# Optimization experiments

Measured on AMD Instinct MI355X. Metric: run time of the kernel, lower is better.

The kernel has to match this reference:

```python
import jax, jax.numpy as jnp
import numpy as np

B, L, C = 8, 256, 64
NEG = -1e30  # large negative instead of -inf to keep grads NaN-free


def setup_inputs() -> dict:
    key = jax.random.key(0)
    k1, k2 = jax.random.split(key)
    scores = jax.random.normal(k1, (B, L, L, C), dtype=jnp.float32)
    lens = jax.random.randint(k2, (B,), 64, L, dtype=jnp.int32)  # sentence lengths in [64, L-1]
    return {"scores": scores, "lens": lens}


def _inside_max(scores, lens):
    """Max-semiring CKY inside pass. scores: [B,L,L,C]; returns logZ per batch [B]."""
    t = jnp.transpose(jnp.max(scores, axis=-1), (1, 2, 0))  # [L,L,B] best label per span
    s0 = jnp.zeros((L, L, B), scores.dtype)                 # chart s[i,j] = best score of span (i,j)
    i = jnp.arange(L)
    j = jnp.arange(L)

    def step(s, w):
        e = jnp.clip(i + w, 0, L - 1)                       # span end, [L]
        k = jnp.clip(i[:, None] + j[None, :], 0, L - 1)     # split points, [L,L]
        left = s[i[:, None], k]                             # s[i, i+j], [L,L,B]
        right = s[k, e[:, None]]                            # s[i+j, i+w], [L,L,B]
        valid = (j[None, :] >= 1) & (j[None, :] < w) & ((i + w) < L)[:, None]
        comb = jnp.max(jnp.where(valid[..., None], left + right, NEG), axis=1)  # [L,B]
        s_l = t[i, e]                                       # label-max span score, [L,B]
        diag = jnp.where(w == 1, s_l, comb + s_l)
        row_ok = ((i + w) < L)[:, None]
        upd = jnp.where(row_ok, diag, s[i, e])
        s = s.at[i, e].set(upd)
        return s, None

    s, _ = jax.lax.scan(step, s0, jnp.arange(1, L))
    lens_c = jnp.clip(lens, 1, L - 1)
    return s[0, lens_c, jnp.arange(B)]                      # logZ (best tree score) per sentence


def reference(scores, lens):
    return _inside_max(scores, lens)
```

## Files before the change

kernel.cpp:

```cpp
#include <hip/hip_runtime.h>

#define LVAL 256
#define T    32
#define ST   36
#define SLAB (T * ST)
#define NB   8
#define NEG  (-1e30f)

#define LDS_FENCE() asm volatile("s_waitcnt lgkmcnt(0)" ::: "memory")

__device__ __forceinline__ size_t sidx(int b, int i, int e) {
    return ((size_t)b << 16) + (i << 8) + e;
}

template<int CTRL>
__device__ __forceinline__ float dpp_max(float v) {
#if __has_builtin(__builtin_amdgcn_mov_dpp)
    int o = __builtin_amdgcn_mov_dpp(__builtin_bit_cast(int, v), CTRL, 0xF, 0xF, true);
    return fmaxf(v, __builtin_bit_cast(float, o));
#else
    return fmaxf(v, __shfl_xor(v, CTRL == 0xB1 ? 1 : 2));
#endif
}

__global__ __launch_bounds__(256) void phase1(const float* __restrict__ scores,
                                              float* __restrict__ s) {
    const int i = blockIdx.x, b = blockIdx.y;
    const int sub = threadIdx.x & 15, slot = threadIdx.x >> 4;
    const float* row = scores + ((((size_t)b * LVAL + i) * LVAL) << 6);
    #pragma unroll 4
    for (int m0 = 0; m0 < LVAL; m0 += 16) {
        const int e = m0 + slot;
        if (e > i) {
            float4 v = *((const float4*)(row + ((size_t)e << 6)) + sub);
            float mx = fmaxf(fmaxf(v.x, v.y), fmaxf(v.z, v.w));
            #pragma unroll
            for (int d = 1; d < 16; d <<= 1) mx = fmaxf(mx, __shfl_xor(mx, d));
            if (sub == 0) s[sidx(b, i, e)] = mx;
        }
    }
}

template<int LP>
__device__ __forceinline__ void diag_step(int lane, int l,
                                          float (*cur)[ST], float (*curT)[ST],
                                          const float (*tb)[ST]) {
    const int cells = T - l;
    const int P = 1 << LP;
    const int c = lane >> LP, p = lane & (P - 1);
    const bool guard = c < cells;
    const int li = guard ? c : 0;
    const int le = guard ? c + l : 0;
    constexpr int NF = 8 >> LP;
    const float tv = tb[li][le];
    float acc = NEG;
    #pragma unroll
    for (int m = 0; m < NF; ++m) {
        const int k0 = 4 * (p + m * P);
        float4 cu = *(const float4*)&cur[li][k0];
        float4 ct = *(const float4*)&curT[le][k0];
        acc = fmaxf(acc, fmaxf(fmaxf(cu.x + ct.x, cu.y + ct.y),
                               fmaxf(cu.z + ct.z, cu.w + ct.w)));
    }
    acc = dpp_max<0xB1>(acc);
    if (LP >= 2) acc = dpp_max<0x4E>(acc);
    const float v = acc + tv;
    if (guard && p == 0) cur[li][le] = v;
    if (guard && p == 1) curT[le][li] = v;
}

__global__ __launch_bounds__(64) void round0(float* __restrict__ s) {
    __shared__ __align__(16) float curS[SLAB], curTS[SLAB], tbS[SLAB];
    float (*cur)[ST]  = (float(*)[ST])curS;
    float (*curT)[ST] = (float(*)[ST])curTS;
    float (*tb)[ST]   = (float(*)[ST])tbS;
    const int bi = blockIdx.x & 7, b = blockIdx.x >> 3;
    const int lane = threadIdx.x;
    const int row = lane >> 1, ch = (lane & 1) * 16;
    const float4 negv = make_float4(NEG, NEG, NEG, NEG);
    #pragma unroll
    for (int j = 0; j < 4; ++j) {
        float4 v = *(const float4*)&s[sidx(b, bi * T + row, bi * T + ch + 4 * j)];
        *(float4*)&tb[row][ch + 4 * j]   = v;
        *(float4*)&cur[row][ch + 4 * j]  = negv;
        *(float4*)&curT[row][ch + 4 * j] = negv;
    }
    LDS_FENCE();
    if (lane < T - 1) {
        float v = tb[lane][lane + 1];
        cur[lane][lane + 1] = v;
        curT[lane + 1][lane] = v;
    }
    LDS_FENCE();
    #pragma unroll 1
    for (int l = 2; l < T; ++l) {
        if (T - l <= 16) diag_step<2>(lane, l, cur, curT, tb);
        else             diag_step<1>(lane, l, cur, curT, tb);
        LDS_FENCE();
    }
    #pragma unroll
    for (int j = 0; j < 4; ++j)
        *(float4*)&s[sidx(b, bi * T + row, bi * T + ch + 4 * j)] =
            *(const float4*)&cur[row][ch + 4 * j];
}

template<int LP>
__device__ __forceinline__ void edge_step(int lane, int l, int D,
                                          const float (*Ae)[ST], const float (*BeT)[ST],
                                          float (*cur)[ST], float (*curT)[ST],
                                          const float (*tb)[ST], const float (*pre)[ST]) {
    const int delta = l - (T - 1);
    const int ad = delta < 0 ? -delta : delta;
    const int cells = T - ad;
    const int P = 1 << LP;
    const int c = lane >> LP, p = lane & (P - 1);
    const bool guard = c < cells;
    const int li = guard ? (delta < 0 ? c + ad : c) : 0;
    const int le = guard ? li + delta : 0;
    constexpr int NF = 8 >> LP;
    const float tv = tb[li][le];
    float acc = pre[li][le];
    #pragma unroll
    for (int m = 0; m < NF; ++m) {
        const int k0 = 4 * (p + m * P);
        float4 a  = *(const float4*)&Ae[li][k0];
        float4 ct = *(const float4*)&curT[le][k0];
        float4 cu = *(const float4*)&cur[li][k0];
        float4 bt = *(const float4*)&BeT[le][k0];
        float s0 = fmaxf(fmaxf(a.x + ct.x, a.y + ct.y), fmaxf(a.z + ct.z, a.w + ct.w));
        float s1 = fmaxf(fmaxf(cu.x + bt.x, cu.y + bt.y), fmaxf(cu.z + bt.z, cu.w + bt.w));
        acc = fmaxf(acc, fmaxf(s0, s1));
    }
    acc = dpp_max<0xB1>(acc);
    if (LP >= 2) acc = dpp_max<0x4E>(acc);
    const float v = (D == 1 && l == 0) ? tv : acc + tv;
    if (guard && p == 0) cur[li][le] = v;
    if (guard && p == 1) curT[le][li] = v;
}

__global__ __launch_bounds__(256) void roundD(float* __restrict__ s, int D,
                                              const int* __restrict__ lens,
                                              float* __restrict__ out) {
    __shared__ __align__(16) float smem[14 * SLAB];
    float (*Ae)[ST]   = (float(*)[ST])(smem + 0 * SLAB);
    float (*BeT)[ST]  = (float(*)[ST])(smem + 1 * SLAB);
    float (*cur)[ST]  = (float(*)[ST])(smem + 2 * SLAB);
    float (*curT)[ST] = (float(*)[ST])(smem + 3 * SLAB);
    float (*tb)[ST]   = (float(*)[ST])(smem + 4 * SLAB);
    float (*pre)[ST]  = (float(*)[ST])(smem + 5 * SLAB);
    float* ATb = smem + 6 * SLAB;
    float* BWb = smem + 10 * SLAB;

    const int nbi = NB - D;
    const int b = blockIdx.x / nbi, bi = blockIdx.x % nbi, be = bi + D;
    const int tid = threadIdx.x, wid = tid >> 6, lane = tid & 63;
    const int lr = tid >> 5, lc = tid & 31;
    const int grow = lane >> 1, gc = (lane & 1) * 16;
    const int gly = lane >> 3, glx = lane & 7, r0 = 4 * gly, c0 = 4 * glx;
    const int nw = (D - 1 < 4) ? (D - 1) : 4;
    float (*AT)[ST] = (float(*)[ST])(ATb + wid * SLAB);
    float (*BW)[ST] = (float(*)[ST])(BWb + wid * SLAB);

    float ag[4][4];
    #pragma unroll
    for (int i = 0; i < 4; ++i)
        #pragma unroll
        for (int j = 0; j < 4; ++j) ag[i][j] = NEG;
    for (int K = bi + 1 + wid; K < be; K += 4) {
        #pragma unroll
        for (int j = 0; j < 4; ++j) {
            float4 av = *(const float4*)&s[sidx(b, bi * T + grow, K * T + gc + 4 * j)];
            AT[gc + 4 * j + 0][grow] = av.x;
            AT[gc + 4 * j + 1][grow] = av.y;
            AT[gc + 4 * j + 2][grow] = av.z;
            AT[gc + 4 * j + 3][grow] = av.w;
            float4 bv = *(const float4*)&s[sidx(b, K * T + grow, be * T + gc + 4 * j)];
            *(float4*)&BW[grow][gc + 4 * j] = bv;
        }
        LDS_FENCE();
        #pragma unroll 4
        for (int k = 0; k < T; ++k) {
            float4 a4 = *(const float4*)&AT[k][r0];
            float4 b4 = *(const float4*)&BW[k][c0];
            const float aa[4] = {a4.x, a4.y, a4.z, a4.w};
            const float bb[4] = {b4.x, b4.y, b4.z, b4.w};
            #pragma unroll
            for (int i = 0; i < 4; ++i)
                #pragma unroll
                for (int j = 0; j < 4; ++j)
                    ag[i][j] = fmaxf(ag[i][j], aa[i] + bb[j]);
        }
        LDS_FENCE();
    }
    if (wid < nw) {
        #pragma unroll
        for (int i = 0; i < 4; ++i)
            *(float4*)&AT[r0 + i][c0] = make_float4(ag[i][0], ag[i][1], ag[i][2], ag[i][3]);
    }
    #pragma unroll
    for (int r = 0; r < 4; ++r) {
        const int row = lr + 8 * r;
        float va = s[sidx(b, bi * T + row, bi * T + lc)];
        Ae[row][lc] = (lc > row) ? va : NEG;
        float vb = s[sidx(b, be * T + row, be * T + lc)];
        BeT[lc][row] = (row < lc) ? vb : NEG;
        tb[row][lc] = s[sidx(b, bi * T + row, be * T + lc)];
        cur[row][lc] = NEG;
        curT[row][lc] = NEG;
    }
    __syncthreads();
    #pragma unroll
    for (int r = 0; r < 4; ++r) {
        const int row = lr + 8 * r;
        float v = NEG;
        for (int w2 = 0; w2 < nw; ++w2)
            v = fmaxf(v, ATb[w2 * SLAB + row * ST + lc]);
        pre[row][lc] = v;
    }
    __syncthreads();

    if (wid == 0) {
        #pragma unroll 1
        for (int l = 0; l < 2 * T - 1; ++l) {
            const int ad0 = (l < T - 1) ? (T - 1 - l) : (l - (T - 1));
            if (ad0 >= 16) edge_step<2>(lane, l, D, Ae, BeT, cur, curT, tb, pre);
            else           edge_step<1>(lane, l, D, Ae, BeT, cur, curT, tb, pre);
            LDS_FENCE();
        }
    }
    __syncthreads();
    #pragma unroll
    for (int r = 0; r < 4; ++r)
        s[sidx(b, bi * T + lr + 8 * r, be * T + lc)] = cur[lr + 8 * r][lc];

    if (D == NB - 1 && tid == 0) {
        int len = lens[b];
        len = len < 1 ? 1 : (len > LVAL - 1 ? LVAL - 1 : len);
        out[b] = (len >= (NB - 1) * T) ? cur[0][len - (NB - 1) * T]
                                       : s[sidx(b, 0, len)];
    }
}

extern "C" void kernel_launch(void* const* d_in, const int* in_sizes, int n_in,
                              void* d_out, int out_size, void* d_ws, size_t ws_size,
                              hipStream_t stream) {
    const float* scores = (const float*)d_in[0];
    const int*   lens   = (const int*)d_in[1];
    float*       out    = (float*)d_out;
    float*       s      = (float*)d_ws;

    phase1<<<dim3(LVAL, 8), 256, 0, stream>>>(scores, s);
    round0<<<64, 64, 0, stream>>>(s);
    for (int D = 1; D < NB; ++D)
        roundD<<<(NB - D) * 8, 256, 0, stream>>>(s, D, lens, out);
}
```

Baseline: 354.1 us.

## Fuse DP rounds into one cooperative kernel with grid syncs and trim edge loop

Replaces the round0 kernel and the seven roundD launches with a single cooperative kernel of 64 blocks that runs all rounds and separates them with grid.sync(). This removes per-launch overhead and the inter-kernel gaps in the serial chain of small kernels. It also adds a trimmed edge_step variant for early anti-diagonals that reads only the half of the split range known to be non-NEG, cutting LDS reads. The trade-off is that a cooperative launch needs every block resident at once, and blocks with no work in later rounds still wait at each grid barrier.

```diff
diff --git a/kernel.cpp b/kernel.cpp
--- a/kernel.cpp
+++ b/kernel.cpp
@@ -1,4 +1,7 @@
 #include <hip/hip_runtime.h>
+#include <hip/hip_cooperative_groups.h>
+
+namespace cg = cooperative_groups;
 
 #define LVAL 256
 #define T    32
@@ -69,42 +72,7 @@
     if (guard && p == 1) curT[le][li] = v;
 }
 
-__global__ __launch_bounds__(64) void round0(float* __restrict__ s) {
-    __shared__ __align__(16) float curS[SLAB], curTS[SLAB], tbS[SLAB];
-    float (*cur)[ST]  = (float(*)[ST])curS;
-    float (*curT)[ST] = (float(*)[ST])curTS;
-    float (*tb)[ST]   = (float(*)[ST])tbS;
-    const int bi = blockIdx.x & 7, b = blockIdx.x >> 3;
-    const int lane = threadIdx.x;
-    const int row = lane >> 1, ch = (lane & 1) * 16;
-    const float4 negv = make_float4(NEG, NEG, NEG, NEG);
-    #pragma unroll
-    for (int j = 0; j < 4; ++j) {
-        float4 v = *(const float4*)&s[sidx(b, bi * T + row, bi * T + ch + 4 * j)];
-        *(float4*)&tb[row][ch + 4 * j]   = v;
-        *(float4*)&cur[row][ch + 4 * j]  = negv;
-        *(float4*)&curT[row][ch + 4 * j] = negv;
-    }
-    LDS_FENCE();
-    if (lane < T - 1) {
-        float v = tb[lane][lane + 1];
-        cur[lane][lane + 1] = v;
-        curT[lane + 1][lane] = v;
-    }
-    LDS_FENCE();
-    #pragma unroll 1
-    for (int l = 2; l < T; ++l) {
-        if (T - l <= 16) diag_step<2>(lane, l, cur, curT, tb);
-        else             diag_step<1>(lane, l, cur, curT, tb);
-        LDS_FENCE();
-    }
-    #pragma unroll
-    for (int j = 0; j < 4; ++j)
-        *(float4*)&s[sidx(b, bi * T + row, bi * T + ch + 4 * j)] =
-            *(const float4*)&cur[row][ch + 4 * j];
-}
-
-template<int LP>
+template<int LP, int TRIM>
 __device__ __forceinline__ void edge_step(int lane, int l, int D,
                                           const float (*Ae)[ST], const float (*BeT)[ST],
                                           float (*cur)[ST], float (*curT)[ST],
@@ -117,19 +85,34 @@
     const bool guard = c < cells;
     const int li = guard ? (delta < 0 ? c + ad : c) : 0;
     const int le = guard ? li + delta : 0;
-    constexpr int NF = 8 >> LP;
     const float tv = tb[li][le];
     float acc = pre[li][le];
-    #pragma unroll
-    for (int m = 0; m < NF; ++m) {
-        const int k0 = 4 * (p + m * P);
-        float4 a  = *(const float4*)&Ae[li][k0];
-        float4 ct = *(const float4*)&curT[le][k0];
-        float4 cu = *(const float4*)&cur[li][k0];
-        float4 bt = *(const float4*)&BeT[le][k0];
-        float s0 = fmaxf(fmaxf(a.x + ct.x, a.y + ct.y), fmaxf(a.z + ct.z, a.w + ct.w));
-        float s1 = fmaxf(fmaxf(cu.x + bt.x, cu.y + bt.y), fmaxf(cu.z + bt.z, cu.w + bt.w));
-        acc = fmaxf(acc, fmaxf(s0, s1));
+    if (TRIM) {
+        constexpr int NF = 4 >> LP;
+        #pragma unroll
+        for (int m = 0; m < (NF ? NF : 1); ++m) {
+            const int kk = 4 * (p + m * P);
+            float4 a  = *(const float4*)&Ae[li][16 + kk];
+            float4 ct = *(const float4*)&curT[le][16 + kk];
+            float4 cu = *(const float4*)&cur[li][kk];
+            float4 bt = *(const float4*)&BeT[le][kk];
+            float s0 = fmaxf(fmaxf(a.x + ct.x, a.y + ct.y), fmaxf(a.z + ct.z, a.w + ct.w));
+            float s1 = fmaxf(fmaxf(cu.x + bt.x, cu.y + bt.y), fmaxf(cu.z + bt.z, cu.w + bt.w));
+            acc = fmaxf(acc, fmaxf(s0, s1));
+        }
+    } else {
+        constexpr int NF = 8 >> LP;
+        #pragma unroll
+        for (int m = 0; m < NF; ++m) {
+            const int k0 = 4 * (p + m * P);
+            float4 a  = *(const float4*)&Ae[li][k0];
+            float4 ct = *(const float4*)&curT[le][k0];
+            float4 cu = *(const float4*)&cur[li][k0];
+            float4 bt = *(const float4*)&BeT[le][k0];
+            float s0 = fmaxf(fmaxf(a.x + ct.x, a.y + ct.y), fmaxf(a.z + ct.z, a.w + ct.w));
+            float s1 = fmaxf(fmaxf(cu.x + bt.x, cu.y + bt.y), fmaxf(cu.z + bt.z, cu.w + bt.w));
+            acc = fmaxf(acc, fmaxf(s0, s1));
+        }
     }
     acc = dpp_max<0xB1>(acc);
     if (LP >= 2) acc = dpp_max<0x4E>(acc);
@@ -138,9 +121,9 @@
     if (guard && p == 1) curT[le][li] = v;
 }
 
-__global__ __launch_bounds__(256) void roundD(float* __restrict__ s, int D,
-                                              const int* __restrict__ lens,
-                                              float* __restrict__ out) {
+__global__ __launch_bounds__(256)
+void dp_coop(float* __restrict__ s, const int* __restrict__ lens,
+             float* __restrict__ out) {
     __shared__ __align__(16) float smem[14 * SLAB];
     float (*Ae)[ST]   = (float(*)[ST])(smem + 0 * SLAB);
     float (*BeT)[ST]  = (float(*)[ST])(smem + 1 * SLAB);
@@ -151,93 +134,139 @@
     float* ATb = smem + 6 * SLAB;
     float* BWb = smem + 10 * SLAB;
 
-    const int nbi = NB - D;
-    const int b = blockIdx.x / nbi, bi = blockIdx.x % nbi, be = bi + D;
+    cg::grid_group grid = cg::this_grid();
     const int tid = threadIdx.x, wid = tid >> 6, lane = tid & 63;
     const int lr = tid >> 5, lc = tid & 31;
     const int grow = lane >> 1, gc = (lane & 1) * 16;
     const int gly = lane >> 3, glx = lane & 7, r0 = 4 * gly, c0 = 4 * glx;
-    const int nw = (D - 1 < 4) ? (D - 1) : 4;
     float (*AT)[ST] = (float(*)[ST])(ATb + wid * SLAB);
     float (*BW)[ST] = (float(*)[ST])(BWb + wid * SLAB);
 
-    float ag[4][4];
-    #pragma unroll
-    for (int i = 0; i < 4; ++i)
-        #pragma unroll
-        for (int j = 0; j < 4; ++j) ag[i][j] = NEG;
-    for (int K = bi + 1 + wid; K < be; K += 4) {
-        #pragma unroll
-        for (int j = 0; j < 4; ++j) {
-            float4 av = *(const float4*)&s[sidx(b, bi * T + grow, K * T + gc + 4 * j)];
-            AT[gc + 4 * j + 0][grow] = av.x;
-            AT[gc + 4 * j + 1][grow] = av.y;
-            AT[gc + 4 * j + 2][grow] = av.z;
-            AT[gc + 4 * j + 3][grow] = av.w;
-            float4 bv = *(const float4*)&s[sidx(b, K * T + grow, be * T + gc + 4 * j)];
-            *(float4*)&BW[grow][gc + 4 * j] = bv;
-        }
-        LDS_FENCE();
-        #pragma unroll 4
-        for (int k = 0; k < T; ++k) {
-            float4 a4 = *(const float4*)&AT[k][r0];
-            float4 b4 = *(const float4*)&BW[k][c0];
-            const float aa[4] = {a4.x, a4.y, a4.z, a4.w};
-            const float bb[4] = {b4.x, b4.y, b4.z, b4.w};
+    {
+        const int bi = blockIdx.x & 7, b = blockIdx.x >> 3;
+        if (wid == 0) {
+            const int row = lane >> 1, ch = (lane & 1) * 16;
+            const float4 negv = make_float4(NEG, NEG, NEG, NEG);
+            #pragma unroll
+            for (int j = 0; j < 4; ++j) {
+                float4 v = *(const float4*)&s[sidx(b, bi * T + row, bi * T + ch + 4 * j)];
+                *(float4*)&tb[row][ch + 4 * j]   = v;
+                *(float4*)&cur[row][ch + 4 * j]  = negv;
+                *(float4*)&curT[row][ch + 4 * j] = negv;
+            }
+            LDS_FENCE();
+            if (lane < T - 1) {
+                float v = tb[lane][lane + 1];
+                cur[lane][lane + 1] = v;
+                curT[lane + 1][lane] = v;
+            }
+            LDS_FENCE();
+            #pragma unroll 1
+            for (int l = 2; l < T; ++l) {
+                if (T - l <= 16) diag_step<2>(lane, l, cur, curT, tb);
+                else             diag_step<1>(lane, l, cur, curT, tb);
+                LDS_FENCE();
+            }
+            #pragma unroll
+            for (int j = 0; j < 4; ++j)
+                *(float4*)&s[sidx(b, bi * T + row, bi * T + ch + 4 * j)] =
+                    *(const float4*)&cur[row][ch + 4 * j];
+        }
+        __syncthreads();
+    }
+    grid.sync();
+
+    for (int D = 1; D < NB; ++D) {
+        const int nbi = NB - D;
+        if (blockIdx.x < nbi * 8) {
+            const int b = blockIdx.x / nbi, bi = blockIdx.x % nbi, be = bi + D;
+            const int nw = (D - 1 < 4) ? (D - 1) : 4;
+
+            float ag[4][4];
             #pragma unroll
             for (int i = 0; i < 4; ++i)
                 #pragma unroll
-                for (int j = 0; j < 4; ++j)
-                    ag[i][j] = fmaxf(ag[i][j], aa[i] + bb[j]);
-        }
-        LDS_FENCE();
-    }
-    if (wid < nw) {
-        #pragma unroll
-        for (int i = 0; i < 4; ++i)
-            *(float4*)&AT[r0 + i][c0] = make_float4(ag[i][0], ag[i][1], ag[i][2], ag[i][3]);
-    }
-    #pragma unroll
-    for (int r = 0; r < 4; ++r) {
-        const int row = lr + 8 * r;
-        float va = s[sidx(b, bi * T + row, bi * T + lc)];
-        Ae[row][lc] = (lc > row) ? va : NEG;
-        float vb = s[sidx(b, be * T + row, be * T + lc)];
-        BeT[lc][row] = (row < lc) ? vb : NEG;
-        tb[row][lc] = s[sidx(b, bi * T + row, be * T + lc)];
-        cur[row][lc] = NEG;
-        curT[row][lc] = NEG;
-    }
-    __syncthreads();
-    #pragma unroll
-    for (int r = 0; r < 4; ++r) {
-        const int row = lr + 8 * r;
-        float v = NEG;
-        for (int w2 = 0; w2 < nw; ++w2)
-            v = fmaxf(v, ATb[w2 * SLAB + row * ST + lc]);
-        pre[row][lc] = v;
-    }
-    __syncthreads();
-
-    if (wid == 0) {
-        #pragma unroll 1
-        for (int l = 0; l < 2 * T - 1; ++l) {
-            const int ad0 = (l < T - 1) ? (T - 1 - l) : (l - (T - 1));
-            if (ad0 >= 16) edge_step<2>(lane, l, D, Ae, BeT, cur, curT, tb, pre);
-            else           edge_step<1>(lane, l, D, Ae, BeT, cur, curT, tb, pre);
-            LDS_FENCE();
-        }
-    }
-    __syncthreads();
-    #pragma unroll
-    for (int r = 0; r < 4; ++r)
-        s[sidx(b, bi * T + lr + 8 * r, be * T + lc)] = cur[lr + 8 * r][lc];
-
-    if (D == NB - 1 && tid == 0) {
-        int len = lens[b];
-        len = len < 1 ? 1 : (len > LVAL - 1 ? LVAL - 1 : len);
-        out[b] = (len >= (NB - 1) * T) ? cur[0][len - (NB - 1) * T]
-                                       : s[sidx(b, 0, len)];
+                for (int j = 0; j < 4; ++j) ag[i][j] = NEG;
+            for (int K = bi + 1 + wid; K < be; K += 4) {
+                #pragma unroll
+                for (int j = 0; j < 4; ++j) {
+                    float4 av = *(const float4*)&s[sidx(b, bi * T + grow, K * T + gc + 4 * j)];
+                    AT[gc + 4 * j + 0][grow] = av.x;
+                    AT[gc + 4 * j + 1][grow] = av.y;
+                    AT[gc + 4 * j + 2][grow] = av.z;
+                    AT[gc + 4 * j + 3][grow] = av.w;
+                    float4 bv = *(const float4*)&s[sidx(b, K * T + grow, be * T + gc + 4 * j)];
+                    *(float4*)&BW[grow][gc + 4 * j] = bv;
+                }
+                LDS_FENCE();
+                #pragma unroll 4
+                for (int k = 0; k < T; ++k) {
+                    float4 a4 = *(const float4*)&AT[k][r0];
+                    float4 b4 = *(const float4*)&BW[k][c0];
+                    const float aa[4] = {a4.x, a4.y, a4.z, a4.w};
+                    const float bb[4] = {b4.x, b4.y, b4.z, b4.w};
+                    #pragma unroll
+                    for (int i = 0; i < 4; ++i)
+                        #pragma unroll
+                        for (int j = 0; j < 4; ++j)
+                            ag[i][j] = fmaxf(ag[i][j], aa[i] + bb[j]);
+                }
+                LDS_FENCE();
+            }
+            if (wid < nw) {
+                #pragma unroll
+                for (int i = 0; i < 4; ++i)
+                    *(float4*)&AT[r0 + i][c0] =
+                        make_float4(ag[i][0], ag[i][1], ag[i][2], ag[i][3]);
+            }
+            #pragma unroll
+            for (int r = 0; r < 4; ++r) {
+                const int row = lr + 8 * r;
+                float va = s[sidx(b, bi * T + row, bi * T + lc)];
+                Ae[row][lc] = (lc > row) ? va : NEG;
+                float vb = s[sidx(b, be * T + row, be * T + lc)];
+                BeT[lc][row] = (row < lc) ? vb : NEG;
+                tb[row][lc] = s[sidx(b, bi * T + row, be * T + lc)];
+                cur[row][lc] = NEG;
+                curT[row][lc] = NEG;
+            }
+            __syncthreads();
+            #pragma unroll
+            for (int r = 0; r < 4; ++r) {
+                const int row = lr + 8 * r;
+                float v = NEG;
+                for (int w2 = 0; w2 < nw; ++w2)
+                    v = fmaxf(v, ATb[w2 * SLAB + row * ST + lc]);
+                pre[row][lc] = v;
+            }
+            __syncthreads();
+
+            if (wid == 0) {
+                #pragma unroll 1
+                for (int l = 0; l < 2 * T - 1; ++l) {
+                    const int ad0 = (l < T - 1) ? (T - 1 - l) : (l - (T - 1));
+                    if (l < T - 1 && ad0 >= 16)
+                        edge_step<2, 1>(lane, l, D, Ae, BeT, cur, curT, tb, pre);
+                    else if (ad0 >= 16)
+                        edge_step<2, 0>(lane, l, D, Ae, BeT, cur, curT, tb, pre);
+                    else
+                        edge_step<1, 0>(lane, l, D, Ae, BeT, cur, curT, tb, pre);
+                    LDS_FENCE();
+                }
+            }
+            __syncthreads();
+            #pragma unroll
+            for (int r = 0; r < 4; ++r)
+                s[sidx(b, bi * T + lr + 8 * r, be * T + lc)] = cur[lr + 8 * r][lc];
+
+            if (D == NB - 1 && tid == 0) {
+                int len = lens[b];
+                len = len < 1 ? 1 : (len > LVAL - 1 ? LVAL - 1 : len);
+                out[b] = (len >= (NB - 1) * T) ? cur[0][len - (NB - 1) * T]
+                                               : s[sidx(b, 0, len)];
+            }
+        }
+        grid.sync();
     }
 }
 
@@ -250,7 +279,7 @@
     float*       s      = (float*)d_ws;
 
     phase1<<<dim3(LVAL, 8), 256, 0, stream>>>(scores, s);
-    round0<<<64, 64, 0, stream>>>(s);
-    for (int D = 1; D < NB; ++D)
-        roundD<<<(NB - D) * 8, 256, 0, stream>>>(s, D, lens, out);
-}
+
+    void* args[] = {(void*)&s, (void*)&lens, (void*)&out};
+    hipLaunchCooperativeKernel((void*)dp_coop, dim3(64), dim3(256), args, 0, stream);
+}
```

Measured after the change: 409.8 us. +15.8%, slower.
